# Kernel tuning notes

Hardware: AMD Instinct MI355X
Metric: run time of the kernel (lower is better)

Reference implementation:

```python
import jax, jax.numpy as jnp
import numpy as np

B, N_FRAMES, IN_DIM, OUT_NODES, N_CH, K_NEIGH = 16, 128, 256, 512, 8, 32


def setup_inputs() -> dict:
    key = jax.random.key(0)
    k0, k1, k2, k3 = jax.random.split(key, 4)
    # kaiming_uniform(a=sqrt(5)) -> bound = 1/sqrt(fan_in); fan_in = prod of dims[1:] for 3D params
    b_w1 = 1.0 / np.sqrt(IN_DIM * IN_DIM)
    b_w2 = 1.0 / np.sqrt(IN_DIM * OUT_NODES)
    b_qk = 1.0 / np.sqrt(N_FRAMES)
    return {
        "inputs": jax.random.normal(k0, (B, N_FRAMES, IN_DIM), dtype=jnp.float32),
        "w1": jax.random.uniform(k1, (N_FRAMES, IN_DIM, IN_DIM), jnp.float32, -b_w1, b_w1),
        "bias1": jnp.zeros((N_FRAMES, 1, IN_DIM), jnp.float32),
        "w2": jax.random.uniform(k2, (N_FRAMES, IN_DIM, OUT_NODES), jnp.float32, -b_w2, b_w2),
        "bias2": jnp.zeros((N_FRAMES, 1, OUT_NODES), jnp.float32),
        "wqk": jax.random.uniform(k3, (N_FRAMES, 2 * N_CH * N_FRAMES), jnp.float32, -b_qk, b_qk),
    }


def _spec_norm(w):
    # spectral norm per node matrix, detached (torch does this under no_grad on .data)
    s = jnp.linalg.norm(w, ord=2, axis=(1, 2), keepdims=True)  # [N,1,1]
    return jax.lax.stop_gradient(jnp.maximum(s, 1e-6))


def _multi_node_mlp(x, w1, b1, w2, b2):
    w1n = w1 / _spec_norm(w1)
    w2n = w2 / _spec_norm(w2)
    h = jnp.einsum("bnd,nde->bne", x, w1n) + b1[:, 0][None]  # [B,N,in]
    h = jax.nn.gelu(h, approximate=False)
    return jnp.einsum("bnd,ndo->bno", h, w2n) + b2[:, 0][None]  # [B,N,out]


def _norm_edge(e):
    norm_row = e / (e.sum(axis=-1, keepdims=True) + 1e-6)
    norm_col = norm_row / (norm_row.sum(axis=-2, keepdims=True) + 1e-6)
    return jnp.einsum("bcnk,bcmk->bcnm", norm_row, norm_col)


def _edge_layer(x, wqk):
    b, n, f = x.shape
    qk = (x @ wqk).reshape(b, n, 2, N_CH, f)
    q = jnp.transpose(qk[:, :, 0], (0, 2, 1, 3))  # [B,C,n,f]
    k = jnp.transpose(qk[:, :, 1], (0, 2, 1, 3))
    attn = jax.nn.softmax(jnp.einsum("bcnf,bcmf->bcnm", q, k) * (f ** -0.5), axis=-1)
    # clip: per-row top-k of channel-summed (detached) attention
    sum_edge = jax.lax.stop_gradient(attn).sum(axis=1)  # [B,n,n]
    _, top_idx = jax.lax.top_k(sum_edge, min(K_NEIGH, n))  # [B,n,k]
    bi = jnp.arange(b)[:, None, None]
    ri = jnp.arange(n)[None, :, None]
    mask = jnp.zeros((b, n, n), attn.dtype).at[bi, ri, top_idx].set(1.0)
    mask = jnp.maximum(mask, jnp.eye(n, dtype=attn.dtype))[:, None]  # [B,1,n,n]
    return _norm_edge(mask * attn)


def reference(inputs, w1, bias1, w2, bias2, wqk):
    converted = _multi_node_mlp(inputs, w1, bias1, w2, bias2)  # [B,frames,nodes]
    node_features = jnp.transpose(converted, (0, 2, 1))  # [B,nodes,frames]
    edge = _edge_layer(node_features, wqk)  # [B,C,nodes,nodes]
    return node_features, edge
```

## Files before the change

### kernel.cpp

```cpp
#include <hip/hip_runtime.h>
#include <hip/hip_bf16.h>
#include <math.h>

#define NFR 128
#define IND 256
#define ONODES 512

static constexpr float SM_SCALE = 0.08838834764831845f;

typedef __attribute__((ext_vector_type(8))) short bf16x8;
typedef __attribute__((ext_vector_type(4))) float f32x4;
typedef __attribute__((ext_vector_type(8))) unsigned short ushort8;
typedef __attribute__((ext_vector_type(4))) unsigned short ushort4v;

__device__ __forceinline__ unsigned short f2bf(float f){
    unsigned int b = __float_as_uint(f);
    b = (b + 0x7fffu + ((b >> 16) & 1u)) >> 16;
    return (unsigned short)b;
}
__device__ __forceinline__ float bf2f(unsigned short u){
    return __uint_as_float(((unsigned int)u) << 16);
}

__global__ __launch_bounds__(512) void kG(const float* __restrict__ w1, const float* __restrict__ w2,
                                          unsigned short* __restrict__ Gb){
    int m = blockIdx.x;
    const float* W; int K;
    if (m < NFR){ W = w1 + (size_t)m * IND * IND; K = IND; }
    else        { W = w2 + (size_t)(m - NFR) * IND * ONODES; K = ONODES; }
    __shared__ unsigned short Wt[256 * 64];
    int t = threadIdx.x;
    int w = t >> 6, l = t & 63;
    int wr = (w >> 2) * 128, wc = (w & 3) * 64;
    f32x4 acc[8][4] = {};
    int srow = t >> 3, sg = t & 7;
    for (int kb = 0; kb < K; kb += 64){
        __syncthreads();
        #pragma unroll
        for (int i = 0; i < 4; ++i){
            int row = i * 64 + srow;
            int dstg = sg ^ (row & 7);
            const float* src = &W[(size_t)row * K + kb + sg * 8];
            float4 f0 = *(const float4*)src;
            float4 f1 = *(const float4*)(src + 4);
            ushort8 v;
            v[0] = f2bf(f0.x); v[1] = f2bf(f0.y); v[2] = f2bf(f0.z); v[3] = f2bf(f0.w);
            v[4] = f2bf(f1.x); v[5] = f2bf(f1.y); v[6] = f2bf(f1.z); v[7] = f2bf(f1.w);
            *(ushort8*)&Wt[row * 64 + dstg * 8] = v;
        }
        __syncthreads();
        #pragma unroll
        for (int kh = 0; kh < 2; ++kh){
            bf16x8 af[8], bfr[4];
            #pragma unroll
            for (int fi = 0; fi < 8; ++fi){
                int row = wr + fi * 16 + (l & 15);
                int g = (kh * 4 + (l >> 4)) ^ (row & 7);
                af[fi] = *(const bf16x8*)&Wt[row * 64 + g * 8];
            }
            #pragma unroll
            for (int fj = 0; fj < 4; ++fj){
                int row = wc + fj * 16 + (l & 15);
                int g = (kh * 4 + (l >> 4)) ^ (row & 7);
                bfr[fj] = *(const bf16x8*)&Wt[row * 64 + g * 8];
            }
            #pragma unroll
            for (int fi = 0; fi < 8; ++fi)
                #pragma unroll
                for (int fj = 0; fj < 4; ++fj)
                    acc[fi][fj] = __builtin_amdgcn_mfma_f32_16x16x32_bf16(af[fi], bfr[fj], acc[fi][fj], 0, 0, 0);
        }
    }
    unsigned short* Gm = Gb + (size_t)m * 65536;
    #pragma unroll
    for (int fi = 0; fi < 8; ++fi){
        #pragma unroll
        for (int r = 0; r < 4; ++r){
            int n = wr + fi * 16 + (l >> 4) * 4 + r;
            unsigned short* grow = Gm + (size_t)n * 256 + wc + (l & 15);
            #pragma unroll
            for (int fj = 0; fj < 4; ++fj) grow[fj * 16] = f2bf(acc[fi][fj][r]);
        }
    }
}

__global__ __launch_bounds__(512) void kG2(const unsigned short* __restrict__ Gb,
                                           unsigned short* __restrict__ G2b){
    int m = blockIdx.x;
    const unsigned short* Gm = Gb + (size_t)m * 65536;
    __shared__ unsigned short Wt[256 * 64];
    int t = threadIdx.x;
    int w = t >> 6, l = t & 63;
    int wr = (w >> 2) * 128, wc = (w & 3) * 64;
    f32x4 acc[8][4] = {};
    int srow = t >> 3, sg = t & 7;
    for (int kb = 0; kb < 256; kb += 64){
        __syncthreads();
        #pragma unroll
        for (int i = 0; i < 4; ++i){
            int row = i * 64 + srow;
            int dstg = sg ^ (row & 7);
            ushort8 v = *(const ushort8*)&Gm[(size_t)row * 256 + kb + sg * 8];
            *(ushort8*)&Wt[row * 64 + dstg * 8] = v;
        }
        __syncthreads();
        #pragma unroll
        for (int kh = 0; kh < 2; ++kh){
            bf16x8 af[8], bfr[4];
            #pragma unroll
            for (int fi = 0; fi < 8; ++fi){
                int row = wr + fi * 16 + (l & 15);
                int g = (kh * 4 + (l >> 4)) ^ (row & 7);
                af[fi] = *(const bf16x8*)&Wt[row * 64 + g * 8];
            }
            #pragma unroll
            for (int fj = 0; fj < 4; ++fj){
                int row = wc + fj * 16 + (l & 15);
                int g = (kh * 4 + (l >> 4)) ^ (row & 7);
                bfr[fj] = *(const bf16x8*)&Wt[row * 64 + g * 8];
            }
            #pragma unroll
            for (int fi = 0; fi < 8; ++fi)
                #pragma unroll
                for (int fj = 0; fj < 4; ++fj)
                    acc[fi][fj] = __builtin_amdgcn_mfma_f32_16x16x32_bf16(af[fi], bfr[fj], acc[fi][fj], 0, 0, 0);
        }
    }
    unsigned short* Om = G2b + (size_t)m * 65536;
    #pragma unroll
    for (int fi = 0; fi < 8; ++fi){
        #pragma unroll
        for (int r = 0; r < 4; ++r){
            int n = wr + fi * 16 + (l >> 4) * 4 + r;
            unsigned short* grow = Om + (size_t)n * 256 + wc + (l & 15);
            #pragma unroll
            for (int fj = 0; fj < 4; ++fj) grow[fj * 16] = f2bf(acc[fi][fj][r]);
        }
    }
}

__global__ __launch_bounds__(512, 1) void kP3(const float* __restrict__ w1, const float* __restrict__ w2,
                                              const unsigned short* __restrict__ G2b, float* __restrict__ inv_s){
    __shared__ unsigned short XT[43008];
    __shared__ float red[24];
    int m = blockIdx.x, t = threadIdx.x;
    int w = t >> 6, l = t & 63;
    int mrow = l & 15, kq = l >> 4;
    const unsigned short* Gm = G2b + (size_t)m * 65536;
    bf16x8 a0[8], a1[8];
    #pragma unroll
    for (int ks = 0; ks < 8; ++ks){
        a0[ks] = *(const bf16x8*)&Gm[(size_t)(w * 32 + mrow) * 256 + ks * 32 + kq * 8];
        a1[ks] = *(const bf16x8*)&Gm[(size_t)(w * 32 + 16 + mrow) * 256 + ks * 32 + kq * 8];
    }
    #pragma unroll
    for (int ks = 0; ks < 8; ++ks){
        asm volatile("" : "+v"(a0[ks]));
        asm volatile("" : "+v"(a1[ks]));
    }
    if (t < 256){
        unsigned int h = (unsigned int)t * 2654435761u ^ 0x9e3779b9u;
        h ^= h >> 13; h *= 0x85ebca6bu; h ^= h >> 16;
        unsigned short xb = f2bf(0.5f + (float)(h & 0xffffu) * (1.0f / 65536.0f));
        #pragma unroll
        for (int c = 0; c < 16; ++c)
            XT[c * 256 + (t ^ ((c & 7) << 3))] = xb;
    }
    __syncthreads();
    int cur = 0;
    for (int it = 0; it < 64; ++it){
        const unsigned short* Xc = &XT[cur * 4096];
        unsigned short* Xn = &XT[(cur ^ 1) * 4096];
        bf16x8 bq[8];
        #pragma unroll
        for (int ks = 0; ks < 8; ++ks)
            bq[ks] = *(const bf16x8*)&Xc[mrow * 256 + ((ks * 32 + kq * 8) ^ ((mrow & 7) << 3))];
        f32x4 acc0 = {}, acc1 = {};
        #pragma unroll
        for (int ks = 0; ks < 8; ++ks){
            acc0 = __builtin_amdgcn_mfma_f32_16x16x32_bf16(a0[ks], bq[ks], acc0, 0, 0, 0);
            acc1 = __builtin_amdgcn_mfma_f32_16x16x32_bf16(a1[ks], bq[ks], acc1, 0, 0, 0);
        }
        int r0 = w * 32 + kq * 4;
        if ((it & 3) == 3){
            float ss = 0.f;
            if (mrow == 0){
                #pragma unroll
                for (int r = 0; r < 4; ++r) ss += acc0[r] * acc0[r] + acc1[r] * acc1[r];
            }
            #pragma unroll
            for (int off = 1; off < 64; off <<= 1) ss += __shfl_xor(ss, off);
            if (l == 0) red[w] = ss;
            __syncthreads();
            float rs = rsqrtf(red[0] + red[1] + red[2] + red[3] + red[4] + red[5] + red[6] + red[7]);
            ushort4v v0, v1;
            #pragma unroll
            for (int r = 0; r < 4; ++r){ v0[r] = f2bf(acc0[r] * rs); v1[r] = f2bf(acc1[r] * rs); }
            *(ushort4v*)&Xn[mrow * 256 + (r0 ^ ((mrow & 7) << 3))] = v0;
            *(ushort4v*)&Xn[mrow * 256 + ((r0 + 16) ^ ((mrow & 7) << 3))] = v1;
            __syncthreads();
        } else {
            ushort4v v0, v1;
            #pragma unroll
            for (int r = 0; r < 4; ++r){ v0[r] = f2bf(acc0[r] * 65536.0f); v1[r] = f2bf(acc1[r] * 65536.0f); }
            *(ushort4v*)&Xn[mrow * 256 + (r0 ^ ((mrow & 7) << 3))] = v0;
            *(ushort4v*)&Xn[mrow * 256 + ((r0 + 16) ^ ((mrow & 7) << 3))] = v1;
            __syncthreads();
        }
        cur ^= 1;
    }
    const unsigned short* Xf = &XT[cur * 4096];
    const float* W; int K;
    if (m < NFR){ W = w1 + (size_t)m * IND * IND; K = IND; }
    else        { W = w2 + (size_t)(m - NFR) * IND * ONODES; K = ONODES; }
    float zsq = 0.f;
    for (int o = t; o < K; o += 512){
        float z = 0.f;
        for (int d = 0; d < 256; ++d) z += W[(size_t)d * K + o] * bf2f(Xf[d]);
        zsq += z * z;
    }
    #pragma unroll
    for (int off = 1; off < 64; off <<= 1) zsq += __shfl_xor(zsq, off);
    if (l == 0) red[8 + w] = zsq;
    float xsq = 0.f;
    if (t < 256){
        float xd = bf2f(Xf[t]);
        xsq = xd * xd;
    }
    #pragma unroll
    for (int off = 1; off < 64; off <<= 1) xsq += __shfl_xor(xsq, off);
    if (l == 0) red[16 + w] = xsq;
    __syncthreads();
    if (t == 0){
        float num = 0.f, den = 0.f;
        #pragma unroll
        for (int i = 0; i < 8; ++i){ num += red[8 + i]; den += red[16 + i]; }
        float sg = sqrtf(fmaxf(num / fmaxf(den, 1e-20f), 0.f));
        inv_s[m] = 1.0f / fmaxf(sg, 1e-6f);
    }
}

__global__ __launch_bounds__(256) void kMLP(const float* __restrict__ inp, const float* __restrict__ w1,
                                            const float* __restrict__ b1, const float* __restrict__ w2,
                                            const float* __restrict__ b2, const float* __restrict__ inv_s,
                                            float* __restrict__ nf, unsigned short* __restrict__ nfb){
    int n = blockIdx.x >> 1, b0 = (blockIdx.x & 1) * 8, t = threadIdx.x;
    __shared__ float xl[8][IND];
    __shared__ float hl[8][IND];
    float i1 = inv_s[n], i2 = inv_s[NFR + n];
    for (int i = t; i < 8 * IND; i += 256){
        int b = i >> 8, d = i & 255;
        xl[b][d] = inp[(size_t)(b0 + b) * (NFR * IND) + (size_t)n * IND + d];
    }
    __syncthreads();
    const float* W1 = w1 + (size_t)n * IND * IND;
    float acc[8] = {};
    for (int d = 0; d < IND; ++d){
        float w = W1[(size_t)d * IND + t];
        #pragma unroll
        for (int b = 0; b < 8; ++b) acc[b] += xl[b][d] * w;
    }
    float bb = b1[(size_t)n * IND + t];
    #pragma unroll
    for (int b = 0; b < 8; ++b){
        float h = acc[b] * i1 + bb;
        h = 0.5f * h * (1.0f + erff(h * 0.70710678118654752f));
        hl[b][t] = h;
    }
    __syncthreads();
    const float* W2 = w2 + (size_t)n * IND * ONODES;
    float o0[8] = {}, o1[8] = {};
    for (int d = 0; d < IND; ++d){
        float wa = W2[(size_t)d * ONODES + t];
        float wb = W2[(size_t)d * ONODES + t + 256];
        #pragma unroll
        for (int b = 0; b < 8; ++b){ float h = hl[b][d]; o0[b] += h * wa; o1[b] += h * wb; }
    }
    float bb0 = b2[(size_t)n * ONODES + t], bb1 = b2[(size_t)n * ONODES + t + 256];
    #pragma unroll
    for (int b = 0; b < 8; ++b){
        float r0 = o0[b] * i2 + bb0;
        float r1 = o1[b] * i2 + bb1;
        size_t bb_ = (size_t)(b0 + b) * (ONODES * NFR);
        nf[bb_ + (size_t)t * NFR + n]         = r0;
        nf[bb_ + (size_t)(t + 256) * NFR + n] = r1;
        nfb[bb_ + (size_t)t * NFR + n]         = f2bf(r0);
        nfb[bb_ + (size_t)(t + 256) * NFR + n] = f2bf(r1);
    }
}

__global__ __launch_bounds__(256) void kWT(const float* __restrict__ wqk, unsigned short* __restrict__ wqkT){
    int j = blockIdx.x * 256 + threadIdx.x;
    unsigned short* dst = wqkT + (size_t)j * 128;
    #pragma unroll
    for (int fb = 0; fb < 16; ++fb){
        ushort8 v;
        #pragma unroll
        for (int u = 0; u < 8; ++u) v[u] = f2bf(wqk[(size_t)(fb * 8 + u) * 2048 + j]);
        *(ushort8*)&dst[fb * 8] = v;
    }
}

__global__ __launch_bounds__(256) void kQK2(const unsigned short* __restrict__ nfb,
                                            const unsigned short* __restrict__ wqkT,
                                            unsigned short* __restrict__ qb, unsigned short* __restrict__ kb){
    int b = blockIdx.x, rb = blockIdx.y, jt = blockIdx.z;
    int t = threadIdx.x, w = t >> 6, l = t & 63;
    int mrow = l & 15, kq = l >> 4;
    const unsigned short* A = nfb + ((size_t)b * 512 + rb * 64) * 128;
    const unsigned short* B = wqkT + (size_t)(jt * 512 + w * 128) * 128;
    f32x4 acc[4][8];
    #pragma unroll
    for (int fi = 0; fi < 4; ++fi)
        #pragma unroll
        for (int fj = 0; fj < 8; ++fj) acc[fi][fj] = (f32x4){0.f, 0.f, 0.f, 0.f};
    #pragma unroll
    for (int kh = 0; kh < 4; ++kh){
        bf16x8 bfr[8];
        #pragma unroll
        for (int fj = 0; fj < 8; ++fj)
            bfr[fj] = *(const bf16x8*)&B[(size_t)(fj * 16 + mrow) * 128 + kh * 32 + kq * 8];
        #pragma unroll
        for (int fi = 0; fi < 4; ++fi){
            bf16x8 af = *(const bf16x8*)&A[(size_t)(fi * 16 + mrow) * 128 + kh * 32 + kq * 8];
            #pragma unroll
            for (int fj = 0; fj < 8; ++fj)
                acc[fi][fj] = __builtin_amdgcn_mfma_f32_16x16x32_bf16(af, bfr[fj], acc[fi][fj], 0, 0, 0);
        }
    }
    #pragma unroll
    for (int fi = 0; fi < 4; ++fi){
        #pragma unroll
        for (int r = 0; r < 4; ++r){
            int node = rb * 64 + fi * 16 + kq * 4 + r;
            #pragma unroll
            for (int fj = 0; fj < 8; ++fj){
                int j = jt * 512 + w * 128 + fj * 16 + mrow;
                int s = j >> 10, c = (j >> 7) & 7, fc = j & 127;
                unsigned short* dst = (s ? kb : qb) + ((size_t)(b * 8 + c) * 512 + node) * 128 + fc;
                *dst = f2bf(acc[fi][fj][r]);
            }
        }
    }
}

__global__ __launch_bounds__(256) void kS2(const unsigned short* __restrict__ qb,
                                           const unsigned short* __restrict__ kb,
                                           unsigned short* __restrict__ attnb){
    int b = blockIdx.x, c = blockIdx.y, rb = blockIdx.z;
    int t = threadIdx.x, w = t >> 6, l = t & 63;
    int mrow = l & 15, kq = l >> 4;
    size_t bc = (size_t)(b * 8 + c) * 512;
    const unsigned short* Q  = qb + (bc + rb * 64) * 128;
    const unsigned short* Kp = kb + (bc + w * 128) * 128;
    __shared__ float rmax[4][64];
    __shared__ float rsum[4][64];
    f32x4 acc[4][8];
    #pragma unroll
    for (int fi = 0; fi < 4; ++fi)
        #pragma unroll
        for (int fj = 0; fj < 8; ++fj) acc[fi][fj] = (f32x4){0.f, 0.f, 0.f, 0.f};
    #pragma unroll
    for (int kh = 0; kh < 4; ++kh){
        bf16x8 kfr[8];
        #pragma unroll
        for (int fj = 0; fj < 8; ++fj)
            kfr[fj] = *(const bf16x8*)&Kp[(size_t)(fj * 16 + mrow) * 128 + kh * 32 + kq * 8];
        #pragma unroll
        for (int fi = 0; fi < 4; ++fi){
            bf16x8 qf = *(const bf16x8*)&Q[(size_t)(fi * 16 + mrow) * 128 + kh * 32 + kq * 8];
            #pragma unroll
            for (int fj = 0; fj < 8; ++fj)
                acc[fi][fj] = __builtin_amdgcn_mfma_f32_16x16x32_bf16(kfr[fj], qf, acc[fi][fj], 0, 0, 0);
        }
    }
    #pragma unroll
    for (int fi = 0; fi < 4; ++fi){
        float mx = acc[fi][0][0];
        #pragma unroll
        for (int fj = 0; fj < 8; ++fj)
            #pragma unroll
            for (int r = 0; r < 4; ++r) mx = fmaxf(mx, acc[fi][fj][r]);
        mx = fmaxf(mx, __shfl_xor(mx, 16));
        mx = fmaxf(mx, __shfl_xor(mx, 32));
        if (kq == 0) rmax[w][fi * 16 + mrow] = mx;
    }
    __syncthreads();
    #pragma unroll
    for (int fi = 0; fi < 4; ++fi){
        int ql = fi * 16 + mrow;
        float gm = fmaxf(fmaxf(rmax[0][ql], rmax[1][ql]), fmaxf(rmax[2][ql], rmax[3][ql]));
        float s = 0.f;
        #pragma unroll
        for (int fj = 0; fj < 8; ++fj)
            #pragma unroll
            for (int r = 0; r < 4; ++r){
                float p = __expf((acc[fi][fj][r] - gm) * SM_SCALE);
                acc[fi][fj][r] = p;
                s += p;
            }
        s += __shfl_xor(s, 16);
        s += __shfl_xor(s, 32);
        if (kq == 0) rsum[w][ql] = s;
    }
    __syncthreads();
    #pragma unroll
    for (int fi = 0; fi < 4; ++fi){
        int ql = fi * 16 + mrow;
        float inv = 1.0f / (rsum[0][ql] + rsum[1][ql] + rsum[2][ql] + rsum[3][ql]);
        size_t rowb = (bc + rb * 64 + ql) * 512 + w * 128 + kq * 4;
        #pragma unroll
        for (int fj = 0; fj < 8; ++fj){
            ushort4v v;
            #pragma unroll
            for (int r = 0; r < 4; ++r) v[r] = f2bf(acc[fi][fj][r] * inv);
            *(ushort4v*)&attnb[rowb + fj * 16] = v;
        }
    }
}

__global__ __launch_bounds__(256) void kTN(const unsigned short* __restrict__ attnb, unsigned short* __restrict__ nrb){
    int b = blockIdx.x >> 9, n = blockIdx.x & 511;
    int t = threadIdx.x, w = t >> 6, lane = t & 63;
    __shared__ unsigned short al[8][512];
    __shared__ unsigned long long keepm[8];
    ushort8* alv = (ushort8*)&al[0][0];
    for (int i = t; i < 512; i += 256){
        int c = i >> 6, o = i & 63;
        alv[i] = *(const ushort8*)&attnb[((size_t)(b * 8 + c) * 512 + n) * 512 + o * 8];
    }
    __syncthreads();
    if (w == 0){
        unsigned int vb[8];
        #pragma unroll
        for (int j = 0; j < 8; ++j){
            float s = 0.f;
            #pragma unroll
            for (int c = 0; c < 8; ++c) s += bf2f(al[c][j * 64 + lane]);
            vb[j] = __float_as_uint(s);
        }
        unsigned int T = 0u;
        for (int bit = 31; bit >= 0; --bit){
            unsigned int cand = T | (1u << bit);
            int cnt = 0;
            #pragma unroll
            for (int j = 0; j < 8; ++j) cnt += __popcll(__ballot(vb[j] >= cand));
            if (cnt >= 32) T = cand;
        }
        int cntgt = 0;
        #pragma unroll
        for (int j = 0; j < 8; ++j) cntgt += __popcll(__ballot(vb[j] > T));
        int need = 32 - cntgt;
        unsigned long long lmask = (1ull << lane) - 1ull;
        int run = 0;
        #pragma unroll
        for (int j = 0; j < 8; ++j){
            bool eq = (vb[j] == T);
            unsigned long long eqm = __ballot(eq);
            int rank = run + __popcll(eqm & lmask);
            bool kv = (vb[j] > T) || (eq && rank < need);
            unsigned long long km = __ballot(kv);
            if (lane == 0) keepm[j] = km;
            run += __popcll(eqm);
        }
    }
    __syncthreads();
    #pragma unroll
    for (int cc = 0; cc < 2; ++cc){
        int c = w * 2 + cc;
        float e[8]; float rs = 0.f;
        #pragma unroll
        for (int j = 0; j < 8; ++j){
            float a = bf2f(al[c][j * 64 + lane]);
            bool keep = ((keepm[j] >> lane) & 1ull) || (j * 64 + lane == n);
            e[j] = keep ? a : 0.0f;
            rs += e[j];
        }
        #pragma unroll
        for (int off = 1; off < 64; off <<= 1) rs += __shfl_xor(rs, off);
        float inv = 1.0f / (rs + 1e-6f);
        size_t base = ((size_t)(b * 8 + c) * 512 + n) * 512;
        #pragma unroll
        for (int j = 0; j < 8; ++j) nrb[base + j * 64 + lane] = f2bf(e[j] * inv);
    }
}

__global__ __launch_bounds__(1024) void kC(const unsigned short* __restrict__ nrb, float* __restrict__ cs){
    int b = blockIdx.x, c = blockIdx.y, t = threadIdx.x;
    int mm = t & 511, nh = t >> 9;
    const unsigned short* Mp = nrb + (size_t)(b * 8 + c) * 262144;
    float s = 0.f;
    for (int n = nh * 256; n < nh * 256 + 256; ++n) s += bf2f(Mp[(size_t)n * 512 + mm]);
    __shared__ float red[1024];
    red[t] = s;
    __syncthreads();
    if (t < 512) cs[(size_t)(b * 8 + c) * 512 + t] = red[t] + red[t + 512];
}

__global__ __launch_bounds__(256) void kF(const unsigned short* __restrict__ S, const float* __restrict__ cs,
                                          float* __restrict__ oe){
    int b = blockIdx.x, c = blockIdx.y, tz = blockIdx.z;
    int nb = (tz >> 2) * 128, mb = (tz & 3) * 128;
    size_t bc = (size_t)(b * 8 + c) * 512;
    const unsigned short* M = S + bc * 512;
    __shared__ unsigned short At[128 * 64];
    __shared__ unsigned short Bt[128 * 64];
    __shared__ float dl[512];
    int t = threadIdx.x;
    for (int i = t; i < 512; i += 256){ float v = cs[bc + i]; dl[i] = 1.0f / (v + 1e-6f); }
    int w = t >> 6, l = t & 63;
    int wr = (w >> 1) * 64, wc = (w & 1) * 64;
    f32x4 acc[4][4] = {};
    int srow = t >> 3, sg = t & 7;
    int mrow = l & 15, kq = l >> 4;
    __syncthreads();
    for (int kb = 0; kb < 512; kb += 64){
        __syncthreads();
        float4 d0 = *(const float4*)&dl[kb + sg * 8];
        float4 d1 = *(const float4*)&dl[kb + sg * 8 + 4];
        float dv[8] = {d0.x, d0.y, d0.z, d0.w, d1.x, d1.y, d1.z, d1.w};
        #pragma unroll
        for (int i = 0; i < 4; ++i){
            int row = i * 32 + srow;
            int dstg = sg ^ (row & 7);
            ushort8 va = *(const ushort8*)&M[(size_t)(nb + row) * 512 + kb + sg * 8];
            ushort8 vb = *(const ushort8*)&M[(size_t)(mb + row) * 512 + kb + sg * 8];
            ushort8 wa;
            #pragma unroll
            for (int j = 0; j < 8; ++j) wa[j] = f2bf(bf2f(va[j]) * dv[j]);
            *(ushort8*)&At[row * 64 + dstg * 8] = wa;
            *(ushort8*)&Bt[row * 64 + dstg * 8] = vb;
        }
        __syncthreads();
        #pragma unroll
        for (int kh = 0; kh < 2; ++kh){
            bf16x8 af[4], bfr[4];
            #pragma unroll
            for (int fi = 0; fi < 4; ++fi){
                int row = wr + fi * 16 + mrow;
                int g = (kh * 4 + kq) ^ (row & 7);
                af[fi] = *(const bf16x8*)&At[row * 64 + g * 8];
            }
            #pragma unroll
            for (int fj = 0; fj < 4; ++fj){
                int row = wc + fj * 16 + mrow;
                int g = (kh * 4 + kq) ^ (row & 7);
                bfr[fj] = *(const bf16x8*)&Bt[row * 64 + g * 8];
            }
            #pragma unroll
            for (int fi = 0; fi < 4; ++fi)
                #pragma unroll
                for (int fj = 0; fj < 4; ++fj)
                    acc[fi][fj] = __builtin_amdgcn_mfma_f32_16x16x32_bf16(bfr[fj], af[fi], acc[fi][fj], 0, 0, 0);
        }
    }
    #pragma unroll
    for (int fi = 0; fi < 4; ++fi){
        int n = nb + wr + fi * 16 + mrow;
        float* orow = oe + (bc + n) * 512 + mb + wc + kq * 4;
        #pragma unroll
        for (int fj = 0; fj < 4; ++fj)
            *(float4*)&orow[fj * 16] = make_float4(acc[fi][fj][0], acc[fi][fj][1], acc[fi][fj][2], acc[fi][fj][3]);
    }
}

extern "C" void kernel_launch(void* const* d_in, const int* in_sizes, int n_in,
                              void* d_out, int out_size, void* d_ws, size_t ws_size,
                              hipStream_t stream) {
    const float* inp = (const float*)d_in[0];
    const float* w1  = (const float*)d_in[1];
    const float* b1  = (const float*)d_in[2];
    const float* w2  = (const float*)d_in[3];
    const float* b2  = (const float*)d_in[4];
    const float* wqk = (const float*)d_in[5];

    float* out_nf   = (float*)d_out;
    float* out_edge = out_nf + (size_t)16 * 512 * 128;

    char* ws = (char*)d_ws;
    float* inv_s = (float*)ws;
    unsigned short* qb  = (unsigned short*)(ws + 4096);
    unsigned short* kbuf = qb + (size_t)16 * 8 * 512 * 128;
    unsigned short* nrb = qb;
    unsigned short* attnb = (unsigned short*)(ws + 4096 + (size_t)134 * 1024 * 1024);
    unsigned short* Gb  = attnb;
    unsigned short* G2b = Gb + (size_t)256 * 65536;
    float* csum = (float*)(attnb + (size_t)16 * 8 * 512 * 512);
    unsigned short* nfb  = (unsigned short*)(csum + (size_t)16 * 8 * 512);
    unsigned short* wqkT = nfb + (size_t)16 * 512 * 128;

    kG  <<<256, 512, 0, stream>>>(w1, w2, Gb);
    kG2 <<<256, 512, 0, stream>>>(Gb, G2b);
    kP3 <<<256, 512, 0, stream>>>(w1, w2, G2b, inv_s);
    kMLP<<<256, 256, 0, stream>>>(inp, w1, b1, w2, b2, inv_s, out_nf, nfb);
    kWT <<<8, 256, 0, stream>>>(wqk, wqkT);
    kQK2<<<dim3(16, 8, 4), 256, 0, stream>>>(nfb, wqkT, qb, kbuf);
    kS2 <<<dim3(16, 8, 8), 256, 0, stream>>>(qb, kbuf, attnb);
    kTN <<<8192, 256, 0, stream>>>(attnb, nrb);
    kC  <<<dim3(16, 8), 1024, 0, stream>>>(nrb, csum);
    kF  <<<dim3(16, 8, 16), 256, 0, stream>>>(nrb, csum, out_edge);
}
```

Baseline: 436.4 us.

## Fuse attention softmax, top-k masking and row normalisation with recompute

Merges the score/softmax kernel, the top-k mask/row-normalise kernel and the column-sum kernel into one kernel per (batch, 32-row block). It computes scores for all 8 channels, accumulates the channel sum in shared memory, selects top-k, then recomputes the QK scores to write the masked row-normalised values and per-block column partial sums. This removes the bf16 attention round trip through global memory and the strided column-sum pass, at the cost of doing the QK matmul twice. Only 256 blocks are launched and each uses large shared memory, which limits occupancy.

Measured after the change: 445.7 us. +2.1%, slower.

```diff
diff --git a/kernel.cpp b/kernel.cpp
--- a/kernel.cpp
+++ b/kernel.cpp
@@ -344,101 +344,94 @@
     }
 }
 
-__global__ __launch_bounds__(256) void kS2(const unsigned short* __restrict__ qb,
-                                           const unsigned short* __restrict__ kb,
-                                           unsigned short* __restrict__ attnb){
-    int b = blockIdx.x, c = blockIdx.y, rb = blockIdx.z;
+__global__ __launch_bounds__(256) void kSTN(const unsigned short* __restrict__ qb,
+                                            const unsigned short* __restrict__ kb,
+                                            unsigned short* __restrict__ nrb,
+                                            float* __restrict__ csp){
+    int b = blockIdx.x, rb = blockIdx.y;
     int t = threadIdx.x, w = t >> 6, l = t & 63;
     int mrow = l & 15, kq = l >> 4;
-    size_t bc = (size_t)(b * 8 + c) * 512;
-    const unsigned short* Q  = qb + (bc + rb * 64) * 128;
-    const unsigned short* Kp = kb + (bc + w * 128) * 128;
-    __shared__ float rmax[4][64];
-    __shared__ float rsum[4][64];
-    f32x4 acc[4][8];
-    #pragma unroll
-    for (int fi = 0; fi < 4; ++fi)
-        #pragma unroll
-        for (int fj = 0; fj < 8; ++fj) acc[fi][fj] = (f32x4){0.f, 0.f, 0.f, 0.f};
-    #pragma unroll
-    for (int kh = 0; kh < 4; ++kh){
-        bf16x8 kfr[8];
-        #pragma unroll
-        for (int fj = 0; fj < 8; ++fj)
-            kfr[fj] = *(const bf16x8*)&Kp[(size_t)(fj * 16 + mrow) * 128 + kh * 32 + kq * 8];
-        #pragma unroll
-        for (int fi = 0; fi < 4; ++fi){
-            bf16x8 qf = *(const bf16x8*)&Q[(size_t)(fi * 16 + mrow) * 128 + kh * 32 + kq * 8];
-            #pragma unroll
-            for (int fj = 0; fj < 8; ++fj)
-                acc[fi][fj] = __builtin_amdgcn_mfma_f32_16x16x32_bf16(kfr[fj], qf, acc[fi][fj], 0, 0, 0);
-        }
-    }
-    #pragma unroll
-    for (int fi = 0; fi < 4; ++fi){
-        float mx = acc[fi][0][0];
-        #pragma unroll
-        for (int fj = 0; fj < 8; ++fj)
-            #pragma unroll
-            for (int r = 0; r < 4; ++r) mx = fmaxf(mx, acc[fi][fj][r]);
-        mx = fmaxf(mx, __shfl_xor(mx, 16));
-        mx = fmaxf(mx, __shfl_xor(mx, 32));
-        if (kq == 0) rmax[w][fi * 16 + mrow] = mx;
-    }
+    __shared__ float sums[512 * 33];
+    __shared__ float red1[4][32];
+    __shared__ float red2[4][32];
+    __shared__ float gmL[8][32];
+    __shared__ float giL[8][32];
+    __shared__ unsigned long long keepm[32][8];
+    for (int i = t; i < 512 * 33; i += 256) sums[i] = 0.f;
     __syncthreads();
-    #pragma unroll
-    for (int fi = 0; fi < 4; ++fi){
-        int ql = fi * 16 + mrow;
-        float gm = fmaxf(fmaxf(rmax[0][ql], rmax[1][ql]), fmaxf(rmax[2][ql], rmax[3][ql]));
-        float s = 0.f;
-        #pragma unroll
-        for (int fj = 0; fj < 8; ++fj)
-            #pragma unroll
-            for (int r = 0; r < 4; ++r){
-                float p = __expf((acc[fi][fj][r] - gm) * SM_SCALE);
-                acc[fi][fj][r] = p;
-                s += p;
-            }
-        s += __shfl_xor(s, 16);
-        s += __shfl_xor(s, 32);
-        if (kq == 0) rsum[w][ql] = s;
-    }
-    __syncthreads();
-    #pragma unroll
-    for (int fi = 0; fi < 4; ++fi){
-        int ql = fi * 16 + mrow;
-        float inv = 1.0f / (rsum[0][ql] + rsum[1][ql] + rsum[2][ql] + rsum[3][ql]);
-        size_t rowb = (bc + rb * 64 + ql) * 512 + w * 128 + kq * 4;
-        #pragma unroll
-        for (int fj = 0; fj < 8; ++fj){
-            ushort4v v;
-            #pragma unroll
-            for (int r = 0; r < 4; ++r) v[r] = f2bf(acc[fi][fj][r] * inv);
-            *(ushort4v*)&attnb[rowb + fj * 16] = v;
-        }
-    }
-}
-
-__global__ __launch_bounds__(256) void kTN(const unsigned short* __restrict__ attnb, unsigned short* __restrict__ nrb){
-    int b = blockIdx.x >> 9, n = blockIdx.x & 511;
-    int t = threadIdx.x, w = t >> 6, lane = t & 63;
-    __shared__ unsigned short al[8][512];
-    __shared__ unsigned long long keepm[8];
-    ushort8* alv = (ushort8*)&al[0][0];
-    for (int i = t; i < 512; i += 256){
-        int c = i >> 6, o = i & 63;
-        alv[i] = *(const ushort8*)&attnb[((size_t)(b * 8 + c) * 512 + n) * 512 + o * 8];
-    }
-    __syncthreads();
-    if (w == 0){
+    for (int c = 0; c < 8; ++c){
+        size_t bc = (size_t)(b * 8 + c) * 512;
+        const unsigned short* Q  = qb + (bc + rb * 32) * 128;
+        const unsigned short* Kp = kb + (bc + (size_t)w * 128) * 128;
+        f32x4 acc[2][8];
+        #pragma unroll
+        for (int fi = 0; fi < 2; ++fi)
+            #pragma unroll
+            for (int fj = 0; fj < 8; ++fj) acc[fi][fj] = (f32x4){0.f, 0.f, 0.f, 0.f};
+        #pragma unroll
+        for (int kh = 0; kh < 4; ++kh){
+            bf16x8 kfr[8];
+            #pragma unroll
+            for (int fj = 0; fj < 8; ++fj)
+                kfr[fj] = *(const bf16x8*)&Kp[(size_t)(fj * 16 + mrow) * 128 + kh * 32 + kq * 8];
+            #pragma unroll
+            for (int fi = 0; fi < 2; ++fi){
+                bf16x8 qf = *(const bf16x8*)&Q[(size_t)(fi * 16 + mrow) * 128 + kh * 32 + kq * 8];
+                #pragma unroll
+                for (int fj = 0; fj < 8; ++fj)
+                    acc[fi][fj] = __builtin_amdgcn_mfma_f32_16x16x32_bf16(kfr[fj], qf, acc[fi][fj], 0, 0, 0);
+            }
+        }
+        #pragma unroll
+        for (int fi = 0; fi < 2; ++fi){
+            float mx = acc[fi][0][0];
+            #pragma unroll
+            for (int fj = 0; fj < 8; ++fj)
+                #pragma unroll
+                for (int r = 0; r < 4; ++r) mx = fmaxf(mx, acc[fi][fj][r]);
+            mx = fmaxf(mx, __shfl_xor(mx, 16));
+            mx = fmaxf(mx, __shfl_xor(mx, 32));
+            if (kq == 0) red1[w][fi * 16 + mrow] = mx;
+        }
+        __syncthreads();
+        float gmr[2];
+        #pragma unroll
+        for (int fi = 0; fi < 2; ++fi){
+            int row = fi * 16 + mrow;
+            float gm = fmaxf(fmaxf(red1[0][row], red1[1][row]), fmaxf(red1[2][row], red1[3][row]));
+            gmr[fi] = gm;
+            float s = 0.f;
+            #pragma unroll
+            for (int fj = 0; fj < 8; ++fj)
+                #pragma unroll
+                for (int r = 0; r < 4; ++r){
+                    float p = __expf((acc[fi][fj][r] - gm) * SM_SCALE);
+                    acc[fi][fj][r] = p;
+                    s += p;
+                }
+            s += __shfl_xor(s, 16);
+            s += __shfl_xor(s, 32);
+            if (kq == 0) red2[w][row] = s;
+        }
+        __syncthreads();
+        #pragma unroll
+        for (int fi = 0; fi < 2; ++fi){
+            int row = fi * 16 + mrow;
+            float inv = 1.0f / (red2[0][row] + red2[1][row] + red2[2][row] + red2[3][row]);
+            if (w == 0 && kq == 0){ gmL[c][row] = gmr[fi]; giL[c][row] = inv; }
+            #pragma unroll
+            for (int fj = 0; fj < 8; ++fj)
+                #pragma unroll
+                for (int r = 0; r < 4; ++r)
+                    sums[(w * 128 + fj * 16 + kq * 4 + r) * 33 + row] += acc[fi][fj][r] * inv;
+        }
+        __syncthreads();
+    }
+    for (int rr = 0; rr < 8; ++rr){
+        int row = w * 8 + rr;
         unsigned int vb[8];
         #pragma unroll
-        for (int j = 0; j < 8; ++j){
-            float s = 0.f;
-            #pragma unroll
-            for (int c = 0; c < 8; ++c) s += bf2f(al[c][j * 64 + lane]);
-            vb[j] = __float_as_uint(s);
-        }
+        for (int j = 0; j < 8; ++j) vb[j] = __float_as_uint(sums[(j * 64 + l) * 33 + row]);
         unsigned int T = 0u;
         for (int bit = 31; bit >= 0; --bit){
             unsigned int cand = T | (1u << bit);
@@ -451,7 +444,7 @@
         #pragma unroll
         for (int j = 0; j < 8; ++j) cntgt += __popcll(__ballot(vb[j] > T));
         int need = 32 - cntgt;
-        unsigned long long lmask = (1ull << lane) - 1ull;
+        unsigned long long lmask = (1ull << l) - 1ull;
         int run = 0;
         #pragma unroll
         for (int j = 0; j < 8; ++j){
@@ -460,41 +453,106 @@
             int rank = run + __popcll(eqm & lmask);
             bool kv = (vb[j] > T) || (eq && rank < need);
             unsigned long long km = __ballot(kv);
-            if (lane == 0) keepm[j] = km;
+            if (l == 0) keepm[row][j] = km;
             run += __popcll(eqm);
         }
     }
     __syncthreads();
-    #pragma unroll
-    for (int cc = 0; cc < 2; ++cc){
-        int c = w * 2 + cc;
-        float e[8]; float rs = 0.f;
-        #pragma unroll
-        for (int j = 0; j < 8; ++j){
-            float a = bf2f(al[c][j * 64 + lane]);
-            bool keep = ((keepm[j] >> lane) & 1ull) || (j * 64 + lane == n);
-            e[j] = keep ? a : 0.0f;
-            rs += e[j];
-        }
-        #pragma unroll
-        for (int off = 1; off < 64; off <<= 1) rs += __shfl_xor(rs, off);
-        float inv = 1.0f / (rs + 1e-6f);
-        size_t base = ((size_t)(b * 8 + c) * 512 + n) * 512;
-        #pragma unroll
-        for (int j = 0; j < 8; ++j) nrb[base + j * 64 + lane] = f2bf(e[j] * inv);
-    }
-}
-
-__global__ __launch_bounds__(1024) void kC(const unsigned short* __restrict__ nrb, float* __restrict__ cs){
-    int b = blockIdx.x, c = blockIdx.y, t = threadIdx.x;
-    int mm = t & 511, nh = t >> 9;
-    const unsigned short* Mp = nrb + (size_t)(b * 8 + c) * 262144;
+    for (int c = 0; c < 8; ++c){
+        size_t bc = (size_t)(b * 8 + c) * 512;
+        const unsigned short* Q  = qb + (bc + rb * 32) * 128;
+        const unsigned short* Kp = kb + (bc + (size_t)w * 128) * 128;
+        f32x4 acc[2][8];
+        #pragma unroll
+        for (int fi = 0; fi < 2; ++fi)
+            #pragma unroll
+            for (int fj = 0; fj < 8; ++fj) acc[fi][fj] = (f32x4){0.f, 0.f, 0.f, 0.f};
+        #pragma unroll
+        for (int kh = 0; kh < 4; ++kh){
+            bf16x8 kfr[8];
+            #pragma unroll
+            for (int fj = 0; fj < 8; ++fj)
+                kfr[fj] = *(const bf16x8*)&Kp[(size_t)(fj * 16 + mrow) * 128 + kh * 32 + kq * 8];
+            #pragma unroll
+            for (int fi = 0; fi < 2; ++fi){
+                bf16x8 qf = *(const bf16x8*)&Q[(size_t)(fi * 16 + mrow) * 128 + kh * 32 + kq * 8];
+                #pragma unroll
+                for (int fj = 0; fj < 8; ++fj)
+                    acc[fi][fj] = __builtin_amdgcn_mfma_f32_16x16x32_bf16(kfr[fj], qf, acc[fi][fj], 0, 0, 0);
+            }
+        }
+        #pragma unroll
+        for (int fi = 0; fi < 2; ++fi){
+            int row = fi * 16 + mrow;
+            float gm = gmL[c][row], inv = giL[c][row];
+            float s = 0.f;
+            #pragma unroll
+            for (int fj = 0; fj < 8; ++fj)
+                #pragma unroll
+                for (int r = 0; r < 4; ++r){
+                    float p = __expf((acc[fi][fj][r] - gm) * SM_SCALE) * inv;
+                    int mg = w * 128 + fj * 16 + kq * 4 + r;
+                    bool keep = ((keepm[row][mg >> 6] >> (mg & 63)) & 1ull) || (mg == rb * 32 + row);
+                    p = keep ? p : 0.f;
+                    acc[fi][fj][r] = p;
+                    s += p;
+                }
+            s += __shfl_xor(s, 16);
+            s += __shfl_xor(s, 32);
+            if (kq == 0) red1[w][row] = s;
+        }
+        __syncthreads();
+        float cp[8][4];
+        #pragma unroll
+        for (int fj = 0; fj < 8; ++fj)
+            #pragma unroll
+            for (int r = 0; r < 4; ++r) cp[fj][r] = 0.f;
+        #pragma unroll
+        for (int fi = 0; fi < 2; ++fi){
+            int row = fi * 16 + mrow;
+            float rs = red1[0][row] + red1[1][row] + red1[2][row] + red1[3][row];
+            float ninv = 1.0f / (rs + 1e-6f);
+            size_t base = (bc + rb * 32 + row) * 512 + w * 128 + kq * 4;
+            #pragma unroll
+            for (int fj = 0; fj < 8; ++fj){
+                ushort4v v;
+                #pragma unroll
+                for (int r = 0; r < 4; ++r){
+                    float nv = acc[fi][fj][r] * ninv;
+                    v[r] = f2bf(nv);
+                    cp[fj][r] += nv;
+                }
+                *(ushort4v*)&nrb[base + fj * 16] = v;
+            }
+        }
+        #pragma unroll
+        for (int fj = 0; fj < 8; ++fj)
+            #pragma unroll
+            for (int r = 0; r < 4; ++r){
+                float s = cp[fj][r];
+                s += __shfl_xor(s, 1);
+                s += __shfl_xor(s, 2);
+                s += __shfl_xor(s, 4);
+                s += __shfl_xor(s, 8);
+                cp[fj][r] = s;
+            }
+        if (mrow == 0){
+            float* cb = csp + (((size_t)(b * 8 + c)) * 16 + rb) * 512 + w * 128 + kq * 4;
+            #pragma unroll
+            for (int fj = 0; fj < 8; ++fj)
+                #pragma unroll
+                for (int r = 0; r < 4; ++r) cb[fj * 16 + r] = cp[fj][r];
+        }
+        __syncthreads();
+    }
+}
+
+__global__ __launch_bounds__(512) void kCR(const float* __restrict__ csp, float* __restrict__ cs){
+    int bc = blockIdx.x, m = threadIdx.x;
     float s = 0.f;
-    for (int n = nh * 256; n < nh * 256 + 256; ++n) s += bf2f(Mp[(size_t)n * 512 + mm]);
-    __shared__ float red[1024];
-    red[t] = s;
-    __syncthreads();
-    if (t < 512) cs[(size_t)(b * 8 + c) * 512 + t] = red[t] + red[t + 512];
+    #pragma unroll
+    for (int rb = 0; rb < 16; ++rb) s += csp[(((size_t)bc) * 16 + rb) * 512 + m];
+    cs[(size_t)bc * 512 + m] = s;
 }
 
 __global__ __launch_bounds__(256) void kF(const unsigned short* __restrict__ S, const float* __restrict__ cs,
@@ -579,14 +637,14 @@
 
     char* ws = (char*)d_ws;
     float* inv_s = (float*)ws;
-    unsigned short* qb  = (unsigned short*)(ws + 4096);
+    unsigned short* qb   = (unsigned short*)(ws + 4096);
     unsigned short* kbuf = qb + (size_t)16 * 8 * 512 * 128;
-    unsigned short* nrb = qb;
-    unsigned short* attnb = (unsigned short*)(ws + 4096 + (size_t)134 * 1024 * 1024);
-    unsigned short* Gb  = attnb;
-    unsigned short* G2b = Gb + (size_t)256 * 65536;
-    float* csum = (float*)(attnb + (size_t)16 * 8 * 512 * 512);
-    unsigned short* nfb  = (unsigned short*)(csum + (size_t)16 * 8 * 512);
+    unsigned short* nrb  = kbuf + (size_t)16 * 8 * 512 * 128;
+    unsigned short* Gb   = nrb;
+    unsigned short* G2b  = Gb + (size_t)256 * 65536;
+    float* csum = (float*)(nrb + (size_t)16 * 8 * 512 * 512);
+    float* csp  = csum + (size_t)128 * 512;
+    unsigned short* nfb  = (unsigned short*)(csp + (size_t)128 * 16 * 512);
     unsigned short* wqkT = nfb + (size_t)16 * 512 * 128;
 
     kG  <<<256, 512, 0, stream>>>(w1, w2, Gb);
@@ -595,8 +653,7 @@
     kMLP<<<256, 256, 0, stream>>>(inp, w1, b1, w2, b2, inv_s, out_nf, nfb);
     kWT <<<8, 256, 0, stream>>>(wqk, wqkT);
     kQK2<<<dim3(16, 8, 4), 256, 0, stream>>>(nfb, wqkT, qb, kbuf);
-    kS2 <<<dim3(16, 8, 8), 256, 0, stream>>>(qb, kbuf, attnb);
-    kTN <<<8192, 256, 0, stream>>>(attnb, nrb);
-    kC  <<<dim3(16, 8), 1024, 0, stream>>>(nrb, csum);
+    kSTN<<<dim3(16, 16), 256, 0, stream>>>(qb, kbuf, nrb, csp);
+    kCR <<<128, 512, 0, stream>>>(csp, csum);
     kF  <<<dim3(16, 8, 16), 256, 0, stream>>>(nrb, csum, out_edge);
 }
```
